# Performance work log

Hardware: AMD Instinct MI355X
Metric: run time of the kernel (lower is better)

Reference implementation:

```python
import jax, jax.numpy as jnp
import numpy as np

N, IN_F, OUT_F = 8192, 512, 256
ALPHA = 0.2  # LeakyReLU negative slope
NEG_INF = -9e15


def setup_inputs() -> dict:
    key = jax.random.key(0)
    k1, k2, k3, k4 = jax.random.split(key, 4)
    input = jax.random.normal(k1, (N, IN_F), dtype=jnp.float32)
    adj = jax.random.randint(k2, (N, N), 0, 2, dtype=jnp.int32)
    # Xavier-like scale for params
    W = jax.random.normal(k3, (IN_F, OUT_F), dtype=jnp.float32) * (1.414 * np.sqrt(2.0 / (IN_F + OUT_F)))
    a = jax.random.normal(k4, (2 * OUT_F, 1), dtype=jnp.float32) * (1.414 * np.sqrt(2.0 / (2 * OUT_F + 1)))
    return {"input": input, "adj": adj, "W": W, "a": a}


def reference(input, adj, W, a):
    h = input @ W                                   # [N, F]
    a1, a2 = a[:OUT_F, 0], a[OUT_F:, 0]             # [F], [F]
    # e[i, j] = leakyrelu(h_i . a1 + h_j . a2) -- equivalent to concat+linear
    s1 = h @ a1                                     # [N]
    s2 = h @ a2                                     # [N]
    e = jax.nn.leaky_relu(s1[:, None] + s2[None, :], negative_slope=ALPHA)  # [N, N]
    e = jnp.where(adj > 0, e, NEG_INF)
    attention = jax.nn.softmax(e, axis=1)           # row-wise softmax
    # dropout p=0.0 / eval mode -> identity
    h_prime = attention @ h                          # [N, F]
    return jax.nn.elu(h_prime)                       # concat=True -> elu
```

## Files before the change

kernel.cpp:

```cpp
#include <hip/hip_runtime.h>
#include <stdint.h>

#define N_NODES 8192
#define IN_FEAT 512
#define OUT_FEAT 256
#define LOG2E 1.4426950408889634f

typedef __bf16 b16x8 __attribute__((ext_vector_type(8)));
typedef unsigned short u16x8v __attribute__((ext_vector_type(8)));
typedef float f32x4 __attribute__((ext_vector_type(4)));

static __device__ __forceinline__ unsigned short f2bf(float f) {
    union { float f; uint32_t u; } v; v.f = f;
    uint32_t r = v.u + 0x7FFFu + ((v.u >> 16) & 1u);
    return (unsigned short)(r >> 16);
}

__global__ __launch_bounds__(256) void k0_transpose_w(const float* __restrict__ W,
                                                      unsigned short* __restrict__ Wt) {
    int tid = blockIdx.x * 256 + threadIdx.x;
    int c = tid & (OUT_FEAT - 1);
    int k = tid >> 8;
    Wt[(size_t)c * IN_FEAT + k] = f2bf(W[(size_t)k * OUT_FEAT + c]);
}

__global__ __launch_bounds__(256) void k1_hgemm(const float* __restrict__ input,
                                                const unsigned short* __restrict__ Wt,
                                                const float* __restrict__ a_vec,
                                                unsigned short* __restrict__ hTf,
                                                float* __restrict__ s1_raw,
                                                float* __restrict__ s2_raw) {
    int tid = threadIdx.x;
    int lane = tid & 63;
    int c = lane & 15, g = lane >> 4;
    int r0 = blockIdx.x * 64 + (tid >> 6) * 16;
    f32x4 acc[16];
#pragma unroll
    for (int t = 0; t < 16; ++t) acc[t] = (f32x4){0.f, 0.f, 0.f, 0.f};
    const float* arow = input + (size_t)(r0 + c) * IN_FEAT;
#pragma unroll 1
    for (int kk = 0; kk < IN_FEAT / 32; ++kk) {
        int kb = kk * 32 + 8 * g;
        float4 x0 = *(const float4*)(arow + kb);
        float4 x1 = *(const float4*)(arow + kb + 4);
        u16x8v au;
        au[0] = f2bf(x0.x); au[1] = f2bf(x0.y); au[2] = f2bf(x0.z); au[3] = f2bf(x0.w);
        au[4] = f2bf(x1.x); au[5] = f2bf(x1.y); au[6] = f2bf(x1.z); au[7] = f2bf(x1.w);
        b16x8 af = __builtin_bit_cast(b16x8, au);
#pragma unroll
        for (int t = 0; t < 16; ++t) {
            b16x8 bf = __builtin_bit_cast(b16x8,
                *(const u16x8v*)(Wt + (size_t)(16 * t + c) * IN_FEAT + kb));
            acc[t] = __builtin_amdgcn_mfma_f32_16x16x32_bf16(af, bf, acc[t], 0, 0, 0);
        }
    }
    float a1v[16], a2v[16];
#pragma unroll
    for (int t = 0; t < 16; ++t) {
        a1v[t] = a_vec[16 * t + c];
        a2v[t] = a_vec[OUT_FEAT + 16 * t + c];
    }
#pragma unroll
    for (int r = 0; r < 4; ++r) {
        float s1p = 0.f, s2p = 0.f;
#pragma unroll
        for (int t = 0; t < 16; ++t) { s1p += acc[t][r] * a1v[t]; s2p += acc[t][r] * a2v[t]; }
#pragma unroll
        for (int m = 1; m <= 8; m <<= 1) { s1p += __shfl_xor(s1p, m); s2p += __shfl_xor(s2p, m); }
        if (c == 0) {
            int row = r0 + 4 * g + r;
            s1_raw[row] = s1p;
            s2_raw[row] = s2p;
        }
    }
    int chunk = r0 >> 5;
    int lp = ((r0 & 16) >> 3) + (g >> 1);
    int e0 = 4 * (g & 1);
#pragma unroll
    for (int t = 0; t < 16; ++t) {
        ushort4 pk;
        pk.x = f2bf(acc[t][0]); pk.y = f2bf(acc[t][1]);
        pk.z = f2bf(acc[t][2]); pk.w = f2bf(acc[t][3]);
        *(ushort4*)(hTf + ((size_t)(chunk * 16 + t) * 64 + lp * 16 + c) * 8 + e0) = pk;
    }
}

__global__ __launch_bounds__(256) void k2_prep(const float* __restrict__ s1_raw,
                                               const float* __restrict__ s2_raw,
                                               float* __restrict__ s2k,
                                               float2* __restrict__ row2) {
    __shared__ float red[256];
    int tid = threadIdx.x;
    float m = -3.0e38f;
    for (int j = tid; j < N_NODES; j += 256) m = fmaxf(m, s2_raw[j]);
    red[tid] = m;
    __syncthreads();
    for (int s = 128; s > 0; s >>= 1) {
        if (tid < s) red[tid] = fmaxf(red[tid], red[tid + s]);
        __syncthreads();
    }
    float M2 = red[0];
    int i = blockIdx.x * 256 + tid;
    float s1 = s1_raw[i];
    float u = s1 + M2;
    float mi = fmaxf(u, 0.2f * u);
    row2[i] = make_float2((s1 - mi) * LOG2E, -0.8f * mi * LOG2E);
    s2k[i] = s2_raw[i] * LOG2E;
}

__global__ __launch_bounds__(256, 3) void k3_flash(const int* __restrict__ adj,
                                                   const unsigned short* __restrict__ hTf,
                                                   const float* __restrict__ s2k,
                                                   const float2* __restrict__ row2,
                                                   float* __restrict__ pout,
                                                   float* __restrict__ rowpart) {
    __shared__ __align__(16) unsigned short tiles[2][8192];
    __shared__ uint32_t lmaskD[2][64];
    __shared__ __align__(16) float ls2k[2048];

    int tid = threadIdx.x;
    int w = tid >> 6, lane = tid & 63;
    int c = lane & 15, g = lane >> 4;
    int ch = w & 1, rq = w >> 1;
    int jq = blockIdx.x & 3;
    int rg = blockIdx.x >> 2;
    int rowbase = rg * 64 + rq * 32;

    int mrow = tid >> 2;
    int mg8 = tid & 3;
    const int* adjbase = adj + (size_t)(rg * 64 + mrow) * N_NODES + jq * 2048 + mg8 * 8;

    *(float4*)&ls2k[tid * 8]     = *(const float4*)(s2k + jq * 2048 + tid * 8);
    *(float4*)&ls2k[tid * 8 + 4] = *(const float4*)(s2k + jq * 2048 + tid * 8 + 4);
    {
        int4 v0 = *(const int4*)(adjbase);
        int4 v1 = *(const int4*)(adjbase + 4);
        unsigned b = (unsigned)(v0.x != 0) | ((unsigned)(v0.y != 0) << 1)
                   | ((unsigned)(v0.z != 0) << 2) | ((unsigned)(v0.w != 0) << 3)
                   | ((unsigned)(v1.x != 0) << 4) | ((unsigned)(v1.y != 0) << 5)
                   | ((unsigned)(v1.z != 0) << 6) | ((unsigned)(v1.w != 0) << 7);
        ((unsigned char*)&lmaskD[0][mrow])[mg8] = (unsigned char)b;
    }
    int4 va0 = *(const int4*)(adjbase + 32);
    int4 va1 = *(const int4*)(adjbase + 36);
    {
        int jc = jq * 64;
#pragma unroll
        for (int q = 0; q < 4; ++q) {
            int ti = w * 4 + q;
            const unsigned short* src = hTf + (size_t)jc * 8192 + (size_t)(ti * 64 + lane) * 8;
            __builtin_amdgcn_global_load_lds(
                (const __attribute__((address_space(1))) uint32_t*)src,
                (__attribute__((address_space(3))) uint32_t*)(&tiles[0][ti * 512]), 16, 0, 0);
        }
    }

    float2 rc0 = row2[rowbase + c];
    float2 rc1 = row2[rowbase + 16 + c];
    float a_row0 = rc0.x, m8_0 = rc0.y;
    float a_row1 = rc1.x, m8_1 = rc1.y;

    f32x4 acc0[8], acc1[8];
#pragma unroll
    for (int t = 0; t < 8; ++t) { acc0[t] = (f32x4){0,0,0,0}; acc1[t] = (f32x4){0,0,0,0}; }
    float lacc0 = 0.f, lacc1 = 0.f;

#pragma unroll 2
    for (int kk = 0; kk < 64; ++kk) {
        int cur = kk & 1;
        __syncthreads();

        int4 vb0, vb1;
        if (kk < 62) {
            vb0 = *(const int4*)(adjbase + (kk + 2) * 32);
            vb1 = *(const int4*)(adjbase + (kk + 2) * 32 + 4);
        }
        if (kk < 63) {
            int jc = jq * 64 + kk + 1;
#pragma unroll
            for (int q = 0; q < 4; ++q) {
                int ti = w * 4 + q;
                const unsigned short* src = hTf + (size_t)jc * 8192 + (size_t)(ti * 64 + lane) * 8;
                __builtin_amdgcn_global_load_lds(
                    (const __attribute__((address_space(1))) uint32_t*)src,
                    (__attribute__((address_space(3))) uint32_t*)(&tiles[cur ^ 1][ti * 512]), 16, 0, 0);
            }
        }

        uint32_t md0 = lmaskD[cur][rq * 32 + c];
        uint32_t md1 = lmaskD[cur][rq * 32 + 16 + c];
        uint32_t mb0 = (md0 >> (8 * g)) & 0xFFu;
        uint32_t mb1 = (md1 >> (8 * g)) & 0xFFu;
        const float* sp = &ls2k[kk * 32 + 8 * g];
        float4 s0 = *(const float4*)sp;
        float4 s1v = *(const float4*)(sp + 4);
        float sv[8] = {s0.x, s0.y, s0.z, s0.w, s1v.x, s1v.y, s1v.z, s1v.w};
        b16x8 af0, af1;
#pragma unroll
        for (int e = 0; e < 8; ++e) {
            float va = a_row0 + sv[e];
            float vb = __builtin_fmaf(va, 0.2f, m8_0);
            float p0 = (mb0 & (1u << e)) ? __builtin_amdgcn_exp2f(fmaxf(va, vb)) : 0.f;
            lacc0 += p0;
            af0[e] = (__bf16)p0;
            float vc = a_row1 + sv[e];
            float vd = __builtin_fmaf(vc, 0.2f, m8_1);
            float p1 = (mb1 & (1u << e)) ? __builtin_amdgcn_exp2f(fmaxf(vc, vd)) : 0.f;
            lacc1 += p1;
            af1[e] = (__bf16)p1;
        }

        const unsigned short* tb = &tiles[cur][ch * 8 * 512];
#pragma unroll
        for (int t = 0; t < 8; ++t) {
            b16x8 bf = __builtin_bit_cast(b16x8, *(const u16x8v*)(tb + t * 512 + lane * 8));
            acc0[t] = __builtin_amdgcn_mfma_f32_16x16x32_bf16(af0, bf, acc0[t], 0, 0, 0);
            acc1[t] = __builtin_amdgcn_mfma_f32_16x16x32_bf16(af1, bf, acc1[t], 0, 0, 0);
        }

        if (kk < 63) {
            unsigned b = (unsigned)(va0.x != 0) | ((unsigned)(va0.y != 0) << 1)
                       | ((unsigned)(va0.z != 0) << 2) | ((unsigned)(va0.w != 0) << 3)
                       | ((unsigned)(va1.x != 0) << 4) | ((unsigned)(va1.y != 0) << 5)
                       | ((unsigned)(va1.z != 0) << 6) | ((unsigned)(va1.w != 0) << 7);
            ((unsigned char*)&lmaskD[cur ^ 1][mrow])[mg8] = (unsigned char)b;
            va0 = vb0; va1 = vb1;
        }
    }

    float l0 = lacc0 + __shfl_xor(lacc0, 16); l0 += __shfl_xor(l0, 32);
    float l1 = lacc1 + __shfl_xor(lacc1, 16); l1 += __shfl_xor(l1, 32);
    if (ch == 0 && g == 0) {
        rowpart[jq * N_NODES + rowbase + c] = l0;
        rowpart[jq * N_NODES + rowbase + 16 + c] = l1;
    }

#pragma unroll
    for (int r = 0; r < 4; ++r) {
        int grow0 = rowbase + 4 * g + r;
        int grow1 = grow0 + 16;
#pragma unroll
        for (int t = 0; t < 8; ++t) {
            pout[((size_t)jq * N_NODES + grow0) * OUT_FEAT + ch * 128 + 16 * t + c] = acc0[t][r];
            pout[((size_t)jq * N_NODES + grow1) * OUT_FEAT + ch * 128 + 16 * t + c] = acc1[t][r];
        }
    }
}

__global__ __launch_bounds__(256) void k4_reduce(const float* __restrict__ pout,
                                                 const float* __restrict__ rowpart,
                                                 float* __restrict__ out) {
    int t = blockIdx.x * 256 + threadIdx.x;
    int row = t >> 8;
    float s = 0.f, l = 0.f;
#pragma unroll
    for (int q = 0; q < 4; ++q) {
        s += pout[(size_t)q * N_NODES * OUT_FEAT + t];
        l += rowpart[q * N_NODES + row];
    }
    float inv = (l > 0.f) ? 1.0f / l : 0.f;
    float x = s * inv;
    out[t] = (x > 0.f) ? x : (__builtin_amdgcn_exp2f(x * LOG2E) - 1.0f);
}

extern "C" void kernel_launch(void* const* d_in, const int* in_sizes, int n_in,
                              void* d_out, int out_size, void* d_ws, size_t ws_size,
                              hipStream_t stream) {
    const float* input = (const float*)d_in[0];
    const int* adj = (const int*)d_in[1];
    const float* W = (const float*)d_in[2];
    const float* a_vec = (const float*)d_in[3];
    float* out = (float*)d_out;

    char* ws = (char*)d_ws;
    unsigned short* Wt  = (unsigned short*)(ws);
    unsigned short* hTf = (unsigned short*)(ws + 262144);
    float*  s2k     = (float*)(ws + 4456448);
    float2* row2    = (float2*)(ws + 4489216);
    float*  s1_raw  = (float*)(ws + 4554752);
    float*  s2_raw  = (float*)(ws + 4587520);
    float*  rowpart = (float*)(ws + 13008896);
    float*  pout    = (float*)(ws + 13139968);

    hipLaunchKernelGGL(k0_transpose_w, dim3(512), dim3(256), 0, stream, W, Wt);
    hipLaunchKernelGGL(k1_hgemm, dim3(N_NODES / 64), dim3(256), 0, stream,
                       input, Wt, a_vec, hTf, s1_raw, s2_raw);
    hipLaunchKernelGGL(k2_prep, dim3(32), dim3(256), 0, stream, s1_raw, s2_raw, s2k, row2);
    hipLaunchKernelGGL(k3_flash, dim3(512), dim3(256), 0, stream,
                       adj, hTf, s2k, row2, pout, rowpart);
    hipLaunchKernelGGL(k4_reduce, dim3(N_NODES * OUT_FEAT / 256), dim3(256), 0, stream,
                       pout, rowpart, out);
}
```

Baseline: 174.2 us.

## Replace __syncthreads with partial vmcnt waits and peel last pipeline iterations

Replaces the per-iteration __syncthreads (which drains all outstanding global loads) with an explicit s_waitcnt vmcnt(2) plus s_barrier. The current tile's async global_load_lds then completes while the next adjacency prefetch stays in flight. The last two iterations are peeled so the loop body has no conditionals, and sched_barriers pin the instruction order. The partial wait count relies on the exact issue order of loads and could be fragile if the compiler reorders or splits memory ops.

```diff
diff --git a/kernel.cpp b/kernel.cpp
--- a/kernel.cpp
+++ b/kernel.cpp
@@ -141,8 +141,7 @@
                    | ((unsigned)(v1.z != 0) << 6) | ((unsigned)(v1.w != 0) << 7);
         ((unsigned char*)&lmaskD[0][mrow])[mg8] = (unsigned char)b;
     }
-    int4 va0 = *(const int4*)(adjbase + 32);
-    int4 va1 = *(const int4*)(adjbase + 36);
+    __builtin_amdgcn_sched_barrier(0);
     {
         int jc = jq * 64;
 #pragma unroll
@@ -154,6 +153,14 @@
                 (__attribute__((address_space(3))) uint32_t*)(&tiles[0][ti * 512]), 16, 0, 0);
         }
     }
+    __builtin_amdgcn_sched_barrier(0);
+    int4 va0 = *(const int4*)(adjbase + 32);
+    int4 va1 = *(const int4*)(adjbase + 36);
+    __builtin_amdgcn_sched_barrier(0);
+    asm volatile("s_waitcnt vmcnt(2) lgkmcnt(0)" ::: "memory");
+    __builtin_amdgcn_sched_barrier(0);
+    __builtin_amdgcn_s_barrier();
+    __builtin_amdgcn_sched_barrier(0);
 
     float2 rc0 = row2[rowbase + c];
     float2 rc1 = row2[rowbase + 16 + c];
@@ -165,17 +172,52 @@
     for (int t = 0; t < 8; ++t) { acc0[t] = (f32x4){0,0,0,0}; acc1[t] = (f32x4){0,0,0,0}; }
     float lacc0 = 0.f, lacc1 = 0.f;
 
+#define SCORE_AND_MFMA(CUR, KK)                                                          \
+    {                                                                                    \
+        uint32_t md0 = lmaskD[CUR][rq * 32 + c];                                         \
+        uint32_t md1 = lmaskD[CUR][rq * 32 + 16 + c];                                    \
+        uint32_t mb0 = (md0 >> (8 * g)) & 0xFFu;                                         \
+        uint32_t mb1 = (md1 >> (8 * g)) & 0xFFu;                                         \
+        const float* sp = &ls2k[(KK) * 32 + 8 * g];                                      \
+        float4 s0 = *(const float4*)sp;                                                  \
+        float4 s1v = *(const float4*)(sp + 4);                                           \
+        float sv[8] = {s0.x, s0.y, s0.z, s0.w, s1v.x, s1v.y, s1v.z, s1v.w};              \
+        b16x8 af0, af1;                                                                  \
+        _Pragma("unroll")                                                                \
+        for (int e = 0; e < 8; ++e) {                                                    \
+            float va = a_row0 + sv[e];                                                   \
+            float vb = __builtin_fmaf(va, 0.2f, m8_0);                                   \
+            float p0 = (mb0 & (1u << e)) ? __builtin_amdgcn_exp2f(fmaxf(va, vb)) : 0.f;  \
+            lacc0 += p0;                                                                 \
+            af0[e] = (__bf16)p0;                                                         \
+            float vc = a_row1 + sv[e];                                                   \
+            float vd = __builtin_fmaf(vc, 0.2f, m8_1);                                   \
+            float p1 = (mb1 & (1u << e)) ? __builtin_amdgcn_exp2f(fmaxf(vc, vd)) : 0.f;  \
+            lacc1 += p1;                                                                 \
+            af1[e] = (__bf16)p1;                                                         \
+        }                                                                                \
+        const unsigned short* tb = &tiles[CUR][ch * 8 * 512];                            \
+        _Pragma("unroll")                                                                \
+        for (int t = 0; t < 8; ++t) {                                                    \
+            b16x8 bf = __builtin_bit_cast(b16x8, *(const u16x8v*)(tb + t * 512 + lane * 8)); \
+            acc0[t] = __builtin_amdgcn_mfma_f32_16x16x32_bf16(af0, bf, acc0[t], 0, 0, 0); \
+            acc1[t] = __builtin_amdgcn_mfma_f32_16x16x32_bf16(af1, bf, acc1[t], 0, 0, 0); \
+        }                                                                                \
+    }
+
+#define PACK_NEXT(CURX)                                                                  \
+    {                                                                                    \
+        unsigned b = (unsigned)(va0.x != 0) | ((unsigned)(va0.y != 0) << 1)              \
+                   | ((unsigned)(va0.z != 0) << 2) | ((unsigned)(va0.w != 0) << 3)       \
+                   | ((unsigned)(va1.x != 0) << 4) | ((unsigned)(va1.y != 0) << 5)       \
+                   | ((unsigned)(va1.z != 0) << 6) | ((unsigned)(va1.w != 0) << 7);      \
+        ((unsigned char*)&lmaskD[(CURX) ^ 1][mrow])[mg8] = (unsigned char)b;             \
+    }
+
 #pragma unroll 2
-    for (int kk = 0; kk < 64; ++kk) {
+    for (int kk = 0; kk < 62; ++kk) {
         int cur = kk & 1;
-        __syncthreads();
-
-        int4 vb0, vb1;
-        if (kk < 62) {
-            vb0 = *(const int4*)(adjbase + (kk + 2) * 32);
-            vb1 = *(const int4*)(adjbase + (kk + 2) * 32 + 4);
-        }
-        if (kk < 63) {
+        {
             int jc = jq * 64 + kk + 1;
 #pragma unroll
             for (int q = 0; q < 4; ++q) {
@@ -186,47 +228,39 @@
                     (__attribute__((address_space(3))) uint32_t*)(&tiles[cur ^ 1][ti * 512]), 16, 0, 0);
             }
         }
-
-        uint32_t md0 = lmaskD[cur][rq * 32 + c];
-        uint32_t md1 = lmaskD[cur][rq * 32 + 16 + c];
-        uint32_t mb0 = (md0 >> (8 * g)) & 0xFFu;
-        uint32_t mb1 = (md1 >> (8 * g)) & 0xFFu;
-        const float* sp = &ls2k[kk * 32 + 8 * g];
-        float4 s0 = *(const float4*)sp;
-        float4 s1v = *(const float4*)(sp + 4);
-        float sv[8] = {s0.x, s0.y, s0.z, s0.w, s1v.x, s1v.y, s1v.z, s1v.w};
-        b16x8 af0, af1;
-#pragma unroll
-        for (int e = 0; e < 8; ++e) {
-            float va = a_row0 + sv[e];
-            float vb = __builtin_fmaf(va, 0.2f, m8_0);
-            float p0 = (mb0 & (1u << e)) ? __builtin_amdgcn_exp2f(fmaxf(va, vb)) : 0.f;
-            lacc0 += p0;
-            af0[e] = (__bf16)p0;
-            float vc = a_row1 + sv[e];
-            float vd = __builtin_fmaf(vc, 0.2f, m8_1);
-            float p1 = (mb1 & (1u << e)) ? __builtin_amdgcn_exp2f(fmaxf(vc, vd)) : 0.f;
-            lacc1 += p1;
-            af1[e] = (__bf16)p1;
-        }
-
-        const unsigned short* tb = &tiles[cur][ch * 8 * 512];
-#pragma unroll
-        for (int t = 0; t < 8; ++t) {
-            b16x8 bf = __builtin_bit_cast(b16x8, *(const u16x8v*)(tb + t * 512 + lane * 8));
-            acc0[t] = __builtin_amdgcn_mfma_f32_16x16x32_bf16(af0, bf, acc0[t], 0, 0, 0);
-            acc1[t] = __builtin_amdgcn_mfma_f32_16x16x32_bf16(af1, bf, acc1[t], 0, 0, 0);
-        }
-
-        if (kk < 63) {
-            unsigned b = (unsigned)(va0.x != 0) | ((unsigned)(va0.y != 0) << 1)
-                       | ((unsigned)(va0.z != 0) << 2) | ((unsigned)(va0.w != 0) << 3)
-                       | ((unsigned)(va1.x != 0) << 4) | ((unsigned)(va1.y != 0) << 5)
-                       | ((unsigned)(va1.z != 0) << 6) | ((unsigned)(va1.w != 0) << 7);
-            ((unsigned char*)&lmaskD[cur ^ 1][mrow])[mg8] = (unsigned char)b;
-            va0 = vb0; va1 = vb1;
-        }
-    }
+        __builtin_amdgcn_sched_barrier(0);
+        int4 vb0 = *(const int4*)(adjbase + (kk + 2) * 32);
+        int4 vb1 = *(const int4*)(adjbase + (kk + 2) * 32 + 4);
+        __builtin_amdgcn_sched_barrier(0);
+        SCORE_AND_MFMA(cur, kk)
+        PACK_NEXT(cur)
+        va0 = vb0; va1 = vb1;
+        __builtin_amdgcn_sched_barrier(0);
+        asm volatile("s_waitcnt vmcnt(2) lgkmcnt(0)" ::: "memory");
+        __builtin_amdgcn_sched_barrier(0);
+        __builtin_amdgcn_s_barrier();
+        __builtin_amdgcn_sched_barrier(0);
+    }
+    {
+        int jc = jq * 64 + 63;
+#pragma unroll
+        for (int q = 0; q < 4; ++q) {
+            int ti = w * 4 + q;
+            const unsigned short* src = hTf + (size_t)jc * 8192 + (size_t)(ti * 64 + lane) * 8;
+            __builtin_amdgcn_global_load_lds(
+                (const __attribute__((address_space(1))) uint32_t*)src,
+                (__attribute__((address_space(3))) uint32_t*)(&tiles[1][ti * 512]), 16, 0, 0);
+        }
+        __builtin_amdgcn_sched_barrier(0);
+        SCORE_AND_MFMA(0, 62)
+        PACK_NEXT(0)
+        __builtin_amdgcn_sched_barrier(0);
+        asm volatile("s_waitcnt vmcnt(0) lgkmcnt(0)" ::: "memory");
+        __builtin_amdgcn_sched_barrier(0);
+        __builtin_amdgcn_s_barrier();
+        __builtin_amdgcn_sched_barrier(0);
+    }
+    SCORE_AND_MFMA(1, 63)
 
     float l0 = lacc0 + __shfl_xor(lacc0, 16); l0 += __shfl_xor(l0, 32);
     float l1 = lacc1 + __shfl_xor(lacc1, 16); l1 += __shfl_xor(l1, 32);
@@ -245,6 +279,8 @@
             pout[((size_t)jq * N_NODES + grow1) * OUT_FEAT + ch * 128 + 16 * t + c] = acc1[t][r];
         }
     }
+#undef SCORE_AND_MFMA
+#undef PACK_NEXT
 }
 
 __global__ __launch_bounds__(256) void k4_reduce(const float* __restrict__ pout,
```

After: 168.4 us. -3.4%, faster.
